# Optimization experiments

Measured on AMD Instinct MI355X. Metric: run time of the kernel, lower is better.

## Reference

```python
import jax, jax.numpy as jnp
import numpy as np

B_IMG = 2
N_PROP = 2000
N_GT = 16
C_FEAT = 256
H_FEAT = 128
W_FEAT = 128
IMG = 1024.0
NUM_CLASSES = 2
BG_THRESH = 0.5          # fg==bg==0.5 -> BETWEEN_THRESHOLDS band is empty
BPI = 512                # batch_size_per_image
NUM_POS_MAX = int(BPI * 0.25)
ENC_W = (1.0, 1.0, 1.0, 1.0, 1.0)
SCALE = 1.0 / 8.0        # feature stride
POOL = 7
SR = 2                   # sampling_ratio
BETA = 1.0 / 9.0
HID = 1024


def _make_boxes(key, shape_prefix, img=IMG):
    kc, ks = jax.random.split(key)
    c = jax.random.uniform(kc, shape_prefix + (2,), minval=0.0, maxval=img)
    s = jax.random.uniform(ks, shape_prefix + (2,), minval=20.0, maxval=200.0)
    lo = jnp.clip(c - 0.5 * s, 0.0, img - 2.0)
    hi = jnp.clip(c + 0.5 * s, lo + 1.0, img)
    return jnp.concatenate([lo, hi], axis=-1)  # [.., x1,y1,x2,y2]


def setup_inputs():
    key = jax.random.key(0)
    ks = jax.random.split(key, 12)
    features = jax.random.normal(ks[0], (B_IMG, C_FEAT, H_FEAT, W_FEAT), dtype=jnp.float32)
    proposals = _make_boxes(ks[1], (B_IMG, N_PROP))
    gt_boxes = _make_boxes(ks[2], (B_IMG, N_GT))
    gt_labels = jax.random.randint(ks[3], (B_IMG, N_GT), 1, NUM_CLASSES, dtype=jnp.int32)
    ka, kb, kt = jax.random.split(ks[4], 3)
    a = jax.random.uniform(ka, (B_IMG, N_GT), minval=10.0, maxval=60.0)
    b = jax.random.uniform(kb, (B_IMG, N_GT), minval=5.0, maxval=30.0)
    th = jax.random.uniform(kt, (B_IMG, N_GT), minval=-np.pi / 2, maxval=np.pi / 2)
    exy = 0.5 * (gt_boxes[..., :2] + gt_boxes[..., 2:])
    gt_ellipses = jnp.stack([a, b, exy[..., 0], exy[..., 1], th], axis=-1)
    d_in = C_FEAT * POOL * POOL
    w1 = jax.random.normal(ks[5], (d_in, HID), dtype=jnp.float32) * 0.02
    b1 = jnp.zeros((HID,), jnp.float32)
    w2 = jax.random.normal(ks[6], (HID, HID), dtype=jnp.float32) * 0.02
    b2 = jnp.zeros((HID,), jnp.float32)
    wc = jax.random.normal(ks[7], (HID, NUM_CLASSES), dtype=jnp.float32) * 0.02
    bc = jnp.zeros((NUM_CLASSES,), jnp.float32)
    wr = jax.random.normal(ks[8], (HID, NUM_CLASSES * 6), dtype=jnp.float32) * 0.02
    br = jnp.zeros((NUM_CLASSES * 6,), jnp.float32)
    return dict(features=features, proposals=proposals, gt_boxes=gt_boxes,
                gt_labels=gt_labels, gt_ellipses=gt_ellipses,
                w1=w1, b1=b1, w2=w2, b2=b2, wc=wc, bc=bc, wr=wr, br=br)


def box_iou(b1, b2):  # [G,4], [P,4] -> [G,P]
    a1 = (b1[:, 2] - b1[:, 0]) * (b1[:, 3] - b1[:, 1])
    a2 = (b2[:, 2] - b2[:, 0]) * (b2[:, 3] - b2[:, 1])
    lt = jnp.maximum(b1[:, None, :2], b2[None, :, :2])
    rb = jnp.minimum(b1[:, None, 2:], b2[None, :, 2:])
    wh = jnp.clip(rb - lt, 0.0)
    inter = wh[..., 0] * wh[..., 1]
    return inter / (a1[:, None] + a2[None, :] - inter)


def encode_ellipses(ell, boxes):  # ell [..,5]=(a,b,cx,cy,theta), boxes [..,4] -> [..,6]
    a, b, ex, ey, th = (ell[..., i] for i in range(5))
    w = jnp.maximum(boxes[..., 2] - boxes[..., 0], 1.0)
    h = jnp.maximum(boxes[..., 3] - boxes[..., 1], 1.0)
    cx = 0.5 * (boxes[..., 0] + boxes[..., 2])
    cy = 0.5 * (boxes[..., 1] + boxes[..., 3])
    wx, wy, wa, wb, wt = ENC_W
    dx = wx * (ex - cx) / w
    dy = wy * (ey - cy) / h
    da = wa * jnp.log(jnp.maximum(2.0 * a, 1e-3) / w)
    db = wb * jnp.log(jnp.maximum(2.0 * b, 1e-3) / h)
    return jnp.stack([dx, dy, da, db, wt * jnp.sin(2.0 * th), wt * jnp.cos(2.0 * th)], axis=-1)


def roi_align(fmap, rois):  # [C,H,W], [R,4] -> [R,C,POOL,POOL]
    C, H, W = fmap.shape
    r = rois * SCALE
    x1, y1, x2, y2 = r[:, 0], r[:, 1], r[:, 2], r[:, 3]
    bw = jnp.maximum(x2 - x1, 1.0) / POOL
    bh = jnp.maximum(y2 - y1, 1.0) / POOL
    S = POOL * SR
    off = (jnp.arange(S, dtype=jnp.float32) + 0.5) / SR  # bin-unit sample offsets
    ys = jnp.clip(y1[:, None] + off[None, :] * bh[:, None], 0.0, H - 1.0)  # [R,S]
    xs = jnp.clip(x1[:, None] + off[None, :] * bw[:, None], 0.0, W - 1.0)
    y0 = jnp.clip(jnp.floor(ys), 0, H - 2).astype(jnp.int32)
    x0 = jnp.clip(jnp.floor(xs), 0, W - 2).astype(jnp.int32)
    ly = ys - y0
    lx = xs - x0
    Ya, Yb = y0[:, :, None], (y0 + 1)[:, :, None]  # [R,S,1]
    Xa, Xb = x0[:, None, :], (x0 + 1)[:, None, :]  # [R,1,S]
    v00 = fmap[:, Ya, Xa]; v01 = fmap[:, Ya, Xb]   # [C,R,S,S]
    v10 = fmap[:, Yb, Xa]; v11 = fmap[:, Yb, Xb]
    wy1 = ly[:, :, None]; wy0 = 1.0 - wy1
    wx1 = lx[:, None, :]; wx0 = 1.0 - wx1
    val = v00 * (wy0 * wx0) + v01 * (wy0 * wx1) + v10 * (wy1 * wx0) + v11 * (wy1 * wx1)
    R = rois.shape[0]
    pooled = val.reshape(C, R, POOL, SR, POOL, SR).mean(axis=(3, 5))
    return pooled.transpose(1, 0, 2, 3)


def reference(features, proposals, gt_boxes, gt_labels, gt_ellipses,
              w1, b1, w2, b2, wc, bc, wr, br):
    B = features.shape[0]
    # add_gt_proposals
    props = jnp.concatenate([proposals, gt_boxes], axis=1)            # [B,P,4]
    # assign_targets_to_proposals: IoU + Matcher (fg=bg=0.5)
    iou = jax.vmap(box_iou)(gt_boxes, props)                          # [B,G,P]
    matched_vals = iou.max(axis=1)
    matches = iou.argmax(axis=1)                                      # [B,P]
    lab = jnp.take_along_axis(gt_labels, matches, axis=1)
    lab = jnp.where(matched_vals < BG_THRESH, 0, lab)                 # background
    # BalancedPositiveNegativeSampler (deterministic, fixed-shape):
    # cap positives at NUM_POS_MAX by random rank, fill rest with random negatives
    rand = jax.random.uniform(jax.random.key(42), lab.shape)
    is_pos = lab > 0
    is_neg = lab == 0
    pos_s = jnp.where(is_pos, rand, -1e9)
    rank = jnp.argsort(jnp.argsort(-pos_s, axis=1), axis=1)
    capped = is_pos & (rank < NUM_POS_MAX)
    prio = jnp.where(capped, rand + 2.0, jnp.where(is_neg, rand, -1e9))
    _, idx = jax.lax.top_k(prio, BPI)                                 # [B,512]
    boxes = jnp.take_along_axis(props, idx[..., None], axis=1)        # [B,512,4]
    labels = jnp.take_along_axis(lab, idx, axis=1)                    # [B,512]
    m = jnp.take_along_axis(matches, idx, axis=1)
    ell = jnp.take_along_axis(gt_ellipses, m[..., None], axis=1)      # [B,512,5]
    targets = encode_ellipses(ell, boxes)                             # [B,512,6]
    # RoIAlign + TwoMLPHead + predictor
    pooled = jax.vmap(roi_align)(features, boxes)                     # [B,512,C,7,7]
    N = B * BPI
    x = pooled.reshape(N, -1)
    x = jax.nn.relu(x @ w1 + b1)
    x = jax.nn.relu(x @ w2 + b2)
    logits = x @ wc + bc                                              # [N,2]
    reg = (x @ wr + br).reshape(N, NUM_CLASSES, 6)
    # ellipse_rcnn_loss
    labels_f = labels.reshape(N)
    t = targets.reshape(N, 6)
    ce = -jnp.take_along_axis(jax.nn.log_softmax(logits, axis=-1), labels_f[:, None], axis=1).mean()
    pred = jnp.take_along_axis(reg, labels_f[:, None, None], axis=1)[:, 0]  # [N,6]
    d = jnp.abs(pred - t)
    sl1 = jnp.where(d < BETA, 0.5 * d * d / BETA, d - 0.5 * BETA)
    reg_loss = jnp.sum(sl1 * (labels_f > 0)[:, None].astype(sl1.dtype)) / N
    return jnp.stack([ce, reg_loss])
```

## Files before the change

### kernel.cpp

```cpp
#include <hip/hip_runtime.h>
#include <hip/hip_bf16.h>
#include <math.h>

#define B_IMG   2
#define N_PROP  2000
#define N_GT    16
#define NPROPS  2016
#define C_FEAT  256
#define H_FEAT  128
#define W_FEAT  128
#define HWF     (H_FEAT*W_FEAT)
#define POOL    7
#define BPI     512
#define NPOSMAX 128
#define NSEL    (B_IMG*BPI)
#define K1      (C_FEAT*POOL*POOL)
#define K1P     12800
#define HID     1024
#define NHEAD   14
#define SPLITK1 8
#define SPLITK2 8

typedef short bf16x8f __attribute__((ext_vector_type(8)));
typedef float f32x4f  __attribute__((ext_vector_type(4)));
typedef short short4v __attribute__((ext_vector_type(4)));

__device__ __forceinline__ void threefry2x32(unsigned k0, unsigned k1,
                                             unsigned& x0, unsigned& x1) {
  unsigned ks[3] = {k0, k1, k0 ^ k1 ^ 0x1BD11BDAu};
  const int R0[4] = {13, 15, 26, 6};
  const int R1[4] = {17, 29, 16, 24};
  x0 += ks[0]; x1 += ks[1];
#pragma unroll
  for (int g = 0; g < 5; g++) {
    const int* rot = (g & 1) ? R1 : R0;
#pragma unroll
    for (int r = 0; r < 4; r++) {
      x0 += x1;
      x1 = (x1 << rot[r]) | (x1 >> (32 - rot[r]));
      x1 ^= x0;
    }
    x0 += ks[(g + 1) % 3];
    x1 += ks[(g + 2) % 3] + (unsigned)(g + 1);
  }
}

#define PRE_SAMPLE   2
#define PRE_TRANS    (PRE_SAMPLE + 2048)
#define PRE_CAST1    (PRE_TRANS + 3136)
#define PRE_CAST0    (PRE_CAST1 + 256)
#define PRE_TOTAL    (PRE_CAST0 + 512)

__global__ __launch_bounds__(256) void k_pre(const float* __restrict__ proposals,
                                             const float* __restrict__ gt_boxes,
                                             const int* __restrict__ gt_labels,
                                             const float* __restrict__ features,
                                             const float* __restrict__ w1,
                                             const float* __restrict__ w2,
                                             float* __restrict__ prio,
                                             int* __restrict__ plab,
                                             int* __restrict__ matches,
                                             __hip_bfloat16* __restrict__ featT,
                                             __hip_bfloat16* __restrict__ W1T,
                                             __hip_bfloat16* __restrict__ W2T,
                                             __hip_bfloat16* __restrict__ Xb) {
  __shared__ __align__(16) char smem[20800];
  int bid = blockIdx.x;
  int tid = threadIdx.x;
  if (bid < PRE_SAMPLE) {
    float* rs    = (float*)smem;
    float* pos_r = (float*)(smem + 8064);
    short* pos_i = (short*)(smem + 16128);
    float* gtb   = (float*)(smem + 20160);
    int*   gtl   = (int*)(smem + 20416);
    int*   cnt   = (int*)(smem + 20480);
    int b = bid;
    int base = b * NPROPS;
    if (tid == 0) *cnt = 0;
    if (tid < N_GT * 4) gtb[tid] = gt_boxes[b * N_GT * 4 + tid];
    if (tid < N_GT) gtl[tid] = gt_labels[b * N_GT + tid];
    __syncthreads();
    for (int i = tid; i < NPROPS; i += 256) {
      unsigned x0 = 0u, x1 = (unsigned)(base + i);
      threefry2x32(0u, 42u, x0, x1);
      unsigned bits = x0 ^ x1;
      float r = __uint_as_float((bits >> 9) | 0x3F800000u) - 1.0f;
      rs[i] = r;
      float p0, p1, p2, p3;
      if (i < N_PROP) {
        const float4 v = *(const float4*)(proposals + ((size_t)b * N_PROP + i) * 4);
        p0 = v.x; p1 = v.y; p2 = v.z; p3 = v.w;
      } else {
        const float* g = &gtb[(i - N_PROP) * 4];
        p0 = g[0]; p1 = g[1]; p2 = g[2]; p3 = g[3];
      }
      float a2 = (p2 - p0) * (p3 - p1);
      float best = -1.0f; int bg = 0;
#pragma unroll
      for (int g = 0; g < N_GT; g++) {
        float g0 = gtb[g*4], g1 = gtb[g*4+1], g2 = gtb[g*4+2], g3 = gtb[g*4+3];
        float a1 = (g2 - g0) * (g3 - g1);
        float wx = fmaxf(fminf(g2, p2) - fmaxf(g0, p0), 0.0f);
        float wy = fmaxf(fminf(g3, p3) - fmaxf(g1, p1), 0.0f);
        float inter = wx * wy;
        float iou = inter / (a1 + a2 - inter);
        if (iou > best) { best = iou; bg = g; }
      }
      matches[base + i] = bg;
      int lab = (best < 0.5f) ? 0 : gtl[bg];
      plab[base + i] = lab;
      if (lab > 0) {
        int s = atomicAdd(cnt, 1);
        pos_i[s] = (short)i; pos_r[s] = r;
      }
    }
    __syncthreads();
    int P = *cnt;
    for (int s = tid; s < P; s += 256) {
      int i = pos_i[s]; float ri = pos_r[s];
      int ch = 0;
      for (int j = 0; j < P; j++) {
        float rj = pos_r[j]; int ij = pos_i[j];
        ch += (rj > ri || (rj == ri && ij < i)) ? 1 : 0;
      }
      rs[i] = (ch < NPOSMAX) ? (ri + 2.0f) : -1000000000.0f;
    }
    __syncthreads();
    for (int i = tid; i < NPROPS; i += 256) prio[base + i] = rs[i];
  } else if (bid < PRE_TRANS) {
    float (*tile)[65] = (float(*)[65])smem;
    int t = bid - PRE_SAMPLE;
    int b = t >> 10;
    int rem = t & 1023;
    int c0 = (rem >> 8) * 64;
    int s0 = (rem & 255) * 64;
    const float* src = features + (size_t)b * C_FEAT * HWF;
    __hip_bfloat16* dst = featT + (size_t)b * HWF * C_FEAT;
    int hw4 = (tid & 15) * 4, cr = tid >> 4;
#pragma unroll
    for (int p = 0; p < 4; p++) {
      int c = cr + p * 16;
      float4 v = *(const float4*)(src + (size_t)(c0 + c) * HWF + s0 + hw4);
      tile[hw4 + 0][c] = v.x; tile[hw4 + 1][c] = v.y;
      tile[hw4 + 2][c] = v.z; tile[hw4 + 3][c] = v.w;
    }
    __syncthreads();
    int c4 = (tid & 15) * 4, hr = tid >> 4;
#pragma unroll
    for (int p = 0; p < 4; p++) {
      int hw = hr + p * 16;
      __hip_bfloat16 o[4] = {__float2bfloat16(tile[hw][c4]), __float2bfloat16(tile[hw][c4+1]),
                             __float2bfloat16(tile[hw][c4+2]), __float2bfloat16(tile[hw][c4+3])};
      *(short4v*)(dst + (size_t)(s0 + hw) * C_FEAT + c0 + c4) = *(short4v*)o;
    }
  } else if (bid < PRE_CAST1) {
    float (*tile)[65] = (float(*)[65])smem;
    int t = bid - PRE_TRANS;
    int p = t >> 6;
    int rem = t & 63;
    int c0 = (rem & 3) * 64;
    int n0 = (rem >> 2) * 64;
    int n4 = (tid & 15) * 4, ig = tid >> 4;
#pragma unroll
    for (int i = ig; i < 64; i += 16) {
      float4 v = *(const float4*)(w1 + (size_t)((c0 + i) * 49 + p) * HID + n0 + n4);
      tile[i][n4] = v.x; tile[i][n4 + 1] = v.y;
      tile[i][n4 + 2] = v.z; tile[i][n4 + 3] = v.w;
    }
    __syncthreads();
    int c4 = (tid & 15) * 4;
#pragma unroll
    for (int i = ig; i < 64; i += 16) {
      __hip_bfloat16 o[4] = {__float2bfloat16(tile[c4][i]), __float2bfloat16(tile[c4 + 1][i]),
                             __float2bfloat16(tile[c4 + 2][i]), __float2bfloat16(tile[c4 + 3][i])};
      *(short4v*)(W1T + (size_t)(n0 + i) * K1P + p * 256 + c0 + c4) = *(short4v*)o;
    }
  } else if (bid < PRE_CAST0) {
    float (*tile)[65] = (float(*)[65])smem;
    int t = bid - PRE_CAST1;
    int c0 = (t & 15) * 64;
    int n0 = (t >> 4) * 64;
    int n4 = (tid & 15) * 4, ig = tid >> 4;
#pragma unroll
    for (int i = ig; i < 64; i += 16) {
      float4 v = *(const float4*)(w2 + (size_t)(c0 + i) * HID + n0 + n4);
      tile[i][n4] = v.x; tile[i][n4 + 1] = v.y;
      tile[i][n4 + 2] = v.z; tile[i][n4 + 3] = v.w;
    }
    __syncthreads();
    int c4 = (tid & 15) * 4;
#pragma unroll
    for (int i = ig; i < 64; i += 16) {
      __hip_bfloat16 o[4] = {__float2bfloat16(tile[c4][i]), __float2bfloat16(tile[c4 + 1][i]),
                             __float2bfloat16(tile[c4 + 2][i]), __float2bfloat16(tile[c4 + 3][i])};
      *(short4v*)(W2T + (size_t)(n0 + i) * HID + c0 + c4) = *(short4v*)o;
    }
  } else {
    int t = bid - PRE_CAST0;
    __hip_bfloat16* buf = (t >> 8) ? W1T : Xb;
    int tt = (t & 255) * 256 + tid;
    int row = tt >> 6;
    int col4 = (tt & 63) << 2;
    short4v z = {0, 0, 0, 0};
    *(short4v*)(buf + (size_t)row * K1P + K1 + col4) = z;
  }
}

__global__ __launch_bounds__(256) void k_select(const float* __restrict__ prio,
    const float* __restrict__ proposals, const float* __restrict__ gt_boxes,
    const int* __restrict__ matches, const int* __restrict__ plab,
    const float* __restrict__ gt_ell,
    float* __restrict__ sel_boxes, int* __restrict__ sel_labels,
    float* __restrict__ targets) {
  int tid = threadIdx.x;
  int wave = tid >> 6, lane = tid & 63;
  int b = blockIdx.y;
  int base = b * NPROPS;
  int i = blockIdx.x * 4 + wave;
  float pi = prio[base + i];
  int rank = 0;
  for (int j = lane; j < NPROPS; j += 64) {
    float pj = prio[base + j];
    rank += (pj > pi || (pj == pi && j < i)) ? 1 : 0;
  }
#pragma unroll
  for (int off = 32; off > 0; off >>= 1) rank += __shfl_down(rank, off);
  if (lane != 0 || rank >= BPI) return;
  int slot = b * BPI + rank;
  float p0, p1, p2, p3;
  if (i < N_PROP) {
    const float* p = proposals + ((size_t)b * N_PROP + i) * 4;
    p0 = p[0]; p1 = p[1]; p2 = p[2]; p3 = p[3];
  } else {
    const float* p = gt_boxes + ((size_t)b * N_GT + (i - N_PROP)) * 4;
    p0 = p[0]; p1 = p[1]; p2 = p[2]; p3 = p[3];
  }
  sel_boxes[slot * 4 + 0] = p0;
  sel_boxes[slot * 4 + 1] = p1;
  sel_boxes[slot * 4 + 2] = p2;
  sel_boxes[slot * 4 + 3] = p3;
  int lb = plab[base + i];
  sel_labels[slot] = lb;
  int m = matches[base + i];
  const float* e = gt_ell + ((size_t)b * N_GT + m) * 5;
  float ea = e[0], eb = e[1], ex = e[2], ey = e[3], eth = e[4];
  float w = fmaxf(p2 - p0, 1.0f), h = fmaxf(p3 - p1, 1.0f);
  float cx = 0.5f * (p0 + p2), cy = 0.5f * (p1 + p3);
  float* t = targets + (size_t)slot * 6;
  t[0] = (ex - cx) / w;
  t[1] = (ey - cy) / h;
  t[2] = logf(fmaxf(2.0f * ea, 0.001f) / w);
  t[3] = logf(fmaxf(2.0f * eb, 0.001f) / h);
  t[4] = sinf(2.0f * eth);
  t[5] = cosf(2.0f * eth);
}

__global__ __launch_bounds__(256) void k_roialign(const __hip_bfloat16* __restrict__ featT,
                                                  const float* __restrict__ sel_boxes,
                                                  __hip_bfloat16* __restrict__ X) {
  int n = blockIdx.x;
  int py = blockIdx.y;
  int t = threadIdx.x;
  int lane = t & 63, sub = t >> 6;
  int c = lane << 2;
  int b = n >> 9;
  const float* bx = sel_boxes + (size_t)n * 4;
  float x1 = bx[0] * 0.125f, y1 = bx[1] * 0.125f;
  float x2 = bx[2] * 0.125f, y2 = bx[3] * 0.125f;
  float bw = fmaxf(x2 - x1, 1.0f) / 7.0f;
  float bh = fmaxf(y2 - y1, 1.0f) / 7.0f;
  const __hip_bfloat16* base = featT + (size_t)b * HWF * C_FEAT;
  int y0A[2]; float lyA[2];
#pragma unroll
  for (int sy = 0; sy < 2; sy++) {
    float off = ((float)(py * 2 + sy) + 0.5f) * 0.5f;
    float ys = fminf(fmaxf(y1 + off * bh, 0.0f), 127.0f);
    int y0 = (int)fminf(fmaxf(floorf(ys), 0.0f), 126.0f);
    y0A[sy] = y0; lyA[sy] = ys - (float)y0;
  }
#pragma unroll
  for (int pass = 0; pass < 2; pass++) {
    int px = sub + (pass << 2);
    if (px >= 7) break;
    float acc[4] = {0.0f, 0.0f, 0.0f, 0.0f};
#pragma unroll
    for (int sx = 0; sx < 2; sx++) {
      float off = ((float)(px * 2 + sx) + 0.5f) * 0.5f;
      float xs = fminf(fmaxf(x1 + off * bw, 0.0f), 127.0f);
      int x0 = (int)fminf(fmaxf(floorf(xs), 0.0f), 126.0f);
      float lx = xs - (float)x0;
#pragma unroll
      for (int sy = 0; sy < 2; sy++) {
        int y0 = y0A[sy]; float ly = lyA[sy];
        const __hip_bfloat16* p = base + ((size_t)(y0 * W_FEAT + x0)) * C_FEAT + c;
        short4v s00 = *(const short4v*)p;
        short4v s01 = *(const short4v*)(p + C_FEAT);
        short4v s10 = *(const short4v*)(p + W_FEAT * C_FEAT);
        short4v s11 = *(const short4v*)(p + W_FEAT * C_FEAT + C_FEAT);
        float w00 = (1.0f - ly) * (1.0f - lx), w01 = (1.0f - ly) * lx;
        float w10 = ly * (1.0f - lx), w11 = ly * lx;
#pragma unroll
        for (int q = 0; q < 4; q++) {
          float v00 = __uint_as_float(((unsigned)(unsigned short)s00[q]) << 16);
          float v01 = __uint_as_float(((unsigned)(unsigned short)s01[q]) << 16);
          float v10 = __uint_as_float(((unsigned)(unsigned short)s10[q]) << 16);
          float v11 = __uint_as_float(((unsigned)(unsigned short)s11[q]) << 16);
          acc[q] += v00 * w00 + v01 * w01 + v10 * w10 + v11 * w11;
        }
      }
    }
    __hip_bfloat16 o[4] = {__float2bfloat16(acc[0] * 0.25f), __float2bfloat16(acc[1] * 0.25f),
                           __float2bfloat16(acc[2] * 0.25f), __float2bfloat16(acc[3] * 0.25f)};
    *(short4v*)&X[(size_t)n * K1P + (size_t)(py * 7 + px) * C_FEAT + c] = *(short4v*)o;
  }
}

__device__ __forceinline__ void gld_lds16(const __hip_bfloat16* g, __hip_bfloat16* l) {
  __builtin_amdgcn_global_load_lds(
      (const __attribute__((address_space(1))) void*)g,
      (__attribute__((address_space(3))) void*)l, 16, 0, 0);
}

#define G1_KC   1600
#define G1_NKT  25
#define G1_ABUF 16384
#define G1_BUFE 24576

__global__ __launch_bounds__(512, 1) void k_gemm1(const __hip_bfloat16* __restrict__ A,
                                                  const __hip_bfloat16* __restrict__ BT,
                                                  __hip_bfloat16* __restrict__ Pb) {
  __shared__ __align__(16) __hip_bfloat16 lds[3 * G1_BUFE];
  const int lin = blockIdx.x;
  const int kz = lin >> 5;
  const int q  = lin & 31;
  const int m0 = (q >> 3) * 256;
  const int n0 = (q & 7) * 128;
  const int kbeg = kz * G1_KC;
  const int tid = threadIdx.x;
  const int wave = tid >> 6, lane = tid & 63;
  const int wm = (wave & 3) * 64, wn = (wave >> 2) * 64;
  const int lm = lane & 15, quad = lane >> 4;

  f32x4f acc[4][4] = {};

  auto stage = [&](int kt, int sb) {
    const int kcol = kbeg + kt * 64;
    __hip_bfloat16* lb = lds + sb * G1_BUFE;
#pragma unroll
    for (int u = 0; u < 4; ++u) {
      int idx = tid + u * 512;
      int r = idx >> 3, g = (idx & 7) ^ (r & 7);
      gld_lds16(A + (size_t)(m0 + r) * K1P + kcol + g * 8, lb + idx * 8);
    }
#pragma unroll
    for (int u = 0; u < 2; ++u) {
      int idx = tid + u * 512;
      int r = idx >> 3, g = (idx & 7) ^ (r & 7);
      gld_lds16(BT + (size_t)(n0 + r) * K1P + kcol + g * 8, lb + G1_ABUF + idx * 8);
    }
  };

  stage(0, 0);
  stage(1, 1);
  asm volatile("s_waitcnt vmcnt(6)" ::: "memory");
  __builtin_amdgcn_s_barrier();

  int buf = 0;
  for (int kt = 0; kt < G1_NKT; ++kt) {
    int sb = buf + 2; if (sb >= 3) sb -= 3;
    if (kt + 2 < G1_NKT) stage(kt + 2, sb);
    const __hip_bfloat16* Ab = lds + buf * G1_BUFE;
    const __hip_bfloat16* Bb = Ab + G1_ABUF;
    bf16x8f af[4][2], bf[4][2];
#pragma unroll
    for (int i = 0; i < 4; ++i)
#pragma unroll
      for (int s = 0; s < 2; ++s)
        af[i][s] = *(const bf16x8f*)(Ab + (wm + i * 16 + lm) * 64 +
                                     (((s << 2) + quad) ^ (lm & 7)) * 8);
#pragma unroll
    for (int j = 0; j < 4; ++j)
#pragma unroll
      for (int s = 0; s < 2; ++s)
        bf[j][s] = *(const bf16x8f*)(Bb + (wn + j * 16 + lm) * 64 +
                                     (((s << 2) + quad) ^ (lm & 7)) * 8);
    __builtin_amdgcn_s_setprio(1);
#pragma unroll
    for (int s = 0; s < 2; ++s)
#pragma unroll
      for (int i = 0; i < 4; ++i)
#pragma unroll
        for (int j = 0; j < 4; ++j)
          acc[i][j] = __builtin_amdgcn_mfma_f32_16x16x32_bf16(af[i][s], bf[j][s], acc[i][j], 0, 0, 0);
    __builtin_amdgcn_s_setprio(0);
    if (kt < G1_NKT - 1) {
      if (kt < G1_NKT - 2) asm volatile("s_waitcnt vmcnt(6)" ::: "memory");
      else                 asm volatile("s_waitcnt vmcnt(0)" ::: "memory");
      __builtin_amdgcn_s_barrier();
    }
    buf = (buf == 2) ? 0 : buf + 1;
  }

  int tileoff = ((m0 >> 8) * 8 + (n0 >> 7)) * 32768;
  __hip_bfloat16* dst = Pb + ((size_t)kz << 20) + tileoff + wave * 4096 + lane * 4;
#pragma unroll
  for (int i = 0; i < 4; ++i)
#pragma unroll
    for (int j = 0; j < 4; ++j) {
      __hip_bfloat16 o[4] = {__float2bfloat16(acc[i][j][0]), __float2bfloat16(acc[i][j][1]),
                             __float2bfloat16(acc[i][j][2]), __float2bfloat16(acc[i][j][3])};
      *(short4v*)(dst + (i * 4 + j) * 256) = *(short4v*)o;
    }
}

template <int MODE>
__global__ __launch_bounds__(MODE == 1 ? 512 : 256)
void k_mfma_gemm(const __hip_bfloat16* __restrict__ A,
                 const __hip_bfloat16* __restrict__ BT,
                 __hip_bfloat16* __restrict__ Pb, int K, int KC) {
  const int AM  = (MODE == 1) ? 256 : 128;
  const int TPB = AM * 2;
  __shared__ __align__(16) __hip_bfloat16 As[AM * 32];
  __shared__ __align__(16) __hip_bfloat16 Bs[128 * 32];
  int lin = blockIdx.x;
  int n0, m0, kz;
  if (MODE == 1) {
    int c = lin & 7, h = lin >> 8, qq = (lin >> 3) & 31;
    kz = c + (h << 3);
    n0 = (qq & 7) * 128;
    m0 = (qq >> 3) * 256;
  } else {
    kz = lin & 7;
    int qq = lin >> 3;
    n0 = (qq & 7) * 128;
    m0 = (qq >> 3) * 128;
  }
  int tid = threadIdx.x;
  int kbeg = kz * KC;
  int srow = tid >> 2;
  int scs  = tid & 3;
  int sg   = scs ^ (srow & 3);
  int scol = sg << 3;
  int wave = tid >> 6, lane = tid & 63;
  const int WMW = AM / 64;
  int wm = (wave % WMW) * 64, wn = (wave / WMW) * 64;
  int lm = lane & 15, quad = lane >> 4;
  int fco = ((quad ^ (lm & 3)) << 3);
  f32x4f acc[4][4] = {};
  for (int k0 = kbeg; k0 < kbeg + KC; k0 += 32) {
    __syncthreads();
#pragma unroll
    for (int r0 = 0; r0 < AM; r0 += TPB / 4)
      gld_lds16(A + (size_t)(m0 + r0 + srow) * K + k0 + scol, &As[(r0 + srow) * 32 + scs * 8]);
#pragma unroll
    for (int r0 = 0; r0 < 128; r0 += TPB / 4)
      gld_lds16(BT + (size_t)(n0 + r0 + srow) * K + k0 + scol, &Bs[(r0 + srow) * 32 + scs * 8]);
    __syncthreads();
    bf16x8f af[4], bf[4];
#pragma unroll
    for (int i = 0; i < 4; i++)
      af[i] = *(const bf16x8f*)&As[(wm + i * 16 + lm) * 32 + fco];
#pragma unroll
    for (int j = 0; j < 4; j++)
      bf[j] = *(const bf16x8f*)&Bs[(wn + j * 16 + lm) * 32 + fco];
#pragma unroll
    for (int i = 0; i < 4; i++)
#pragma unroll
      for (int j = 0; j < 4; j++)
        acc[i][j] = __builtin_amdgcn_mfma_f32_16x16x32_bf16(af[i], bf[j], acc[i][j], 0, 0, 0);
  }
  int tileoff = (MODE == 1) ? (((m0 >> 8) * 8 + (n0 >> 7)) * 32768)
                            : (((m0 >> 7) * 8 + (n0 >> 7)) * 16384);
  __hip_bfloat16* dst = Pb + ((size_t)kz << 20) + tileoff + wave * 4096 + lane * 4;
#pragma unroll
  for (int i = 0; i < 4; i++)
#pragma unroll
    for (int j = 0; j < 4; j++) {
      __hip_bfloat16 o[4] = {__float2bfloat16(acc[i][j][0]), __float2bfloat16(acc[i][j][1]),
                             __float2bfloat16(acc[i][j][2]), __float2bfloat16(acc[i][j][3])};
      *(short4v*)(dst + (i * 4 + j) * 256) = *(short4v*)o;
    }
}

__global__ __launch_bounds__(256) void k_reduce16(const __hip_bfloat16* __restrict__ Pb,
                                                  const float* __restrict__ bias,
                                                  __hip_bfloat16* __restrict__ O) {
  int m4 = blockIdx.x >> 2;
  int n  = (blockIdx.x & 3) * 256 + threadIdx.x;
  int m0i = m4 >> 6, wavem = (m4 >> 4) & 3, i = (m4 >> 2) & 3, quad = m4 & 3;
  int n0i = n >> 7, wn = (n >> 6) & 1, j = (n >> 4) & 3, lm = n & 15;
  int wave = wavem + wn * 4;
  int elem = (m0i * 8 + n0i) * 32768 + wave * 4096 + (i * 4 + j) * 256 + (quad * 16 + lm) * 4;
  float s0 = 0.0f, s1 = 0.0f, s2 = 0.0f, s3 = 0.0f;
#pragma unroll
  for (int z = 0; z < SPLITK1; z++) {
    short4v v = *(const short4v*)(Pb + ((size_t)z << 20) + elem);
    s0 += __uint_as_float(((unsigned)(unsigned short)v[0]) << 16);
    s1 += __uint_as_float(((unsigned)(unsigned short)v[1]) << 16);
    s2 += __uint_as_float(((unsigned)(unsigned short)v[2]) << 16);
    s3 += __uint_as_float(((unsigned)(unsigned short)v[3]) << 16);
  }
  float bv = bias[n];
  int m = m4 * 4;
  O[(size_t)(m + 0) * HID + n] = __float2bfloat16(fmaxf(s0 + bv, 0.0f));
  O[(size_t)(m + 1) * HID + n] = __float2bfloat16(fmaxf(s1 + bv, 0.0f));
  O[(size_t)(m + 2) * HID + n] = __float2bfloat16(fmaxf(s2 + bv, 0.0f));
  O[(size_t)(m + 3) * HID + n] = __float2bfloat16(fmaxf(s3 + bv, 0.0f));
}

__global__ __launch_bounds__(256) void k_reduce_head(const __hip_bfloat16* __restrict__ Pb,
                                                     const float* __restrict__ bias,
                                                     const float* __restrict__ wc,
                                                     const float* __restrict__ bc,
                                                     const float* __restrict__ wr,
                                                     const float* __restrict__ br,
                                                     float* __restrict__ Y) {
  __shared__ float part[4][NHEAD];
  int m = blockIdx.x, tid = threadIdx.x;
  int m0i = m >> 7, wavem = (m >> 6) & 1, fi = (m >> 4) & 3, quad = (m >> 2) & 3, r = m & 3;
  float a[NHEAD];
#pragma unroll
  for (int j = 0; j < NHEAD; j++) a[j] = 0.0f;
#pragma unroll
  for (int nn = 0; nn < 4; nn++) {
    int n = nn * 256 + tid;
    int n0i = n >> 7, wn = (n >> 6) & 1, fj = (n >> 4) & 3, lm = n & 15;
    int wave = wavem + wn * 2;
    int elem = (m0i * 8 + n0i) * 16384 + wave * 4096 + (fi * 4 + fj) * 256
             + (quad * 16 + lm) * 4 + r;
    float s = 0.0f;
#pragma unroll
    for (int z = 0; z < SPLITK2; z++)
      s += __uint_as_float(((unsigned)*(const unsigned short*)(Pb + ((size_t)z << 20) + elem)) << 16);
    float hv = fmaxf(s + bias[n], 0.0f);
    float2 wcv = *(const float2*)(wc + n * 2);
    float4 w0 = *(const float4*)(wr + n * 12);
    float4 w1 = *(const float4*)(wr + n * 12 + 4);
    float4 w2 = *(const float4*)(wr + n * 12 + 8);
    a[0] += hv * wcv.x;  a[1] += hv * wcv.y;
    a[2] += hv * w0.x;   a[3] += hv * w0.y;  a[4] += hv * w0.z;  a[5] += hv * w0.w;
    a[6] += hv * w1.x;   a[7] += hv * w1.y;  a[8] += hv * w1.z;  a[9] += hv * w1.w;
    a[10] += hv * w2.x;  a[11] += hv * w2.y; a[12] += hv * w2.z; a[13] += hv * w2.w;
  }
#pragma unroll
  for (int j = 0; j < NHEAD; j++)
#pragma unroll
    for (int off = 32; off > 0; off >>= 1) a[j] += __shfl_down(a[j], off);
  int wave = tid >> 6, lane = tid & 63;
  if (lane == 0)
#pragma unroll
    for (int j = 0; j < NHEAD; j++) part[wave][j] = a[j];
  __syncthreads();
  if (tid < NHEAD) {
    float v = part[0][tid] + part[1][tid] + part[2][tid] + part[3][tid];
    Y[(size_t)m * NHEAD + tid] = v + ((tid < 2) ? bc[tid] : br[tid - 2]);
  }
}

__global__ __launch_bounds__(1024) void k_loss(const float* __restrict__ Y,
                                               const int* __restrict__ sel_labels,
                                               const float* __restrict__ T,
                                               float* __restrict__ out) {
  __shared__ float sc[1024];
  __shared__ float sr[1024];
  int n = threadIdx.x;
  float l0 = Y[(size_t)n * NHEAD + 0], l1 = Y[(size_t)n * NHEAD + 1];
  int lb = sel_labels[n];
  float mx = fmaxf(l0, l1);
  float lse = mx + logf(expf(l0 - mx) + expf(l1 - mx));
  float ce = lse - (lb ? l1 : l0);
  float reg = 0.0f;
  if (lb > 0) {
    const float beta = 1.0f / 9.0f;
    const float* pr = Y + (size_t)n * NHEAD + 2 + lb * 6;
    const float* t = T + (size_t)n * 6;
#pragma unroll
    for (int j = 0; j < 6; j++) {
      float d = fabsf(pr[j] - t[j]);
      reg += (d < beta) ? (0.5f * d * d / beta) : (d - 0.5f * beta);
    }
  }
  sc[n] = ce; sr[n] = reg;
  __syncthreads();
  for (int s = 512; s > 0; s >>= 1) {
    if (n < s) { sc[n] += sc[n + s]; sr[n] += sr[n + s]; }
    __syncthreads();
  }
  if (n == 0) {
    out[0] = sc[0] * (1.0f / 1024.0f);
    out[1] = sr[0] * (1.0f / 1024.0f);
  }
}

extern "C" void kernel_launch(void* const* d_in, const int* in_sizes, int n_in,
                              void* d_out, int out_size, void* d_ws, size_t ws_size,
                              hipStream_t stream) {
  const float* features  = (const float*)d_in[0];
  const float* proposals = (const float*)d_in[1];
  const float* gt_boxes  = (const float*)d_in[2];
  const int*   gt_labels = (const int*)d_in[3];
  const float* gt_ell    = (const float*)d_in[4];
  const float* w1 = (const float*)d_in[5];
  const float* b1 = (const float*)d_in[6];
  const float* w2 = (const float*)d_in[7];
  const float* b2 = (const float*)d_in[8];
  const float* wc = (const float*)d_in[9];
  const float* bc = (const float*)d_in[10];
  const float* wr = (const float*)d_in[11];
  const float* br = (const float*)d_in[12];
  float* out = (float*)d_out;

  char* ws = (char*)d_ws;
  size_t off = 0;
  auto take = [&](size_t bytes) -> void* {
    void* p = ws + off;
    off = (off + bytes + 255) & ~(size_t)255;
    return p;
  };
  __hip_bfloat16* Pb = (__hip_bfloat16*)take((size_t)16 * (1 << 20) * 2);
  __hip_bfloat16* featT = Pb;
  __hip_bfloat16* Xb  = (__hip_bfloat16*)take((size_t)NSEL * K1P * 2);
  float* Y = (float*)Xb;
  __hip_bfloat16* W1T = (__hip_bfloat16*)take((size_t)HID * K1P * 2);
  __hip_bfloat16* W2T = (__hip_bfloat16*)take((size_t)HID * HID * 2);
  __hip_bfloat16* H1b = (__hip_bfloat16*)take((size_t)NSEL * HID * 2);
  int*   matches   = (int*)take((size_t)B_IMG * NPROPS * 4);
  int*   plab      = (int*)take((size_t)B_IMG * NPROPS * 4);
  float* prio      = (float*)take((size_t)B_IMG * NPROPS * 4);
  float* sel_boxes = (float*)take((size_t)NSEL * 4 * 4);
  int*   sel_lab   = (int*)take((size_t)NSEL * 4);
  float* targets   = (float*)take((size_t)NSEL * 6 * 4);

  k_pre<<<PRE_TOTAL, 256, 0, stream>>>(proposals, gt_boxes, gt_labels, features,
                                       w1, w2, prio, plab, matches,
                                       featT, W1T, W2T, Xb);
  k_select<<<dim3(NPROPS / 4, B_IMG), 256, 0, stream>>>(prio, proposals, gt_boxes,
                                                        matches, plab, gt_ell,
                                                        sel_boxes, sel_lab, targets);
  k_roialign<<<dim3(NSEL, POOL), 256, 0, stream>>>(featT, sel_boxes, Xb);

  k_gemm1<<<256, 512, 0, stream>>>(Xb, W1T, Pb);
  k_reduce16<<<1024, 256, 0, stream>>>(Pb, b1, H1b);
  k_mfma_gemm<2><<<512, 256, 0, stream>>>(H1b, W2T, Pb, HID, HID / SPLITK2);
  k_reduce_head<<<1024, 256, 0, stream>>>(Pb, b2, wc, bc, wr, br, Y);

  k_loss<<<1, 1024, 0, stream>>>(Y, sel_lab, targets, out);
}
```

Measured before the change: 245.6 us.

## Widen RoIAlign loads, remap gemm1 block order, fuse loss into head reduce

RoIAlign now has each thread handle 8 channels with 16-byte loads and stores, one pooled column per 32-thread group, instead of two passes of 4 channels. The gemm1 block index mapping is permuted so that consecutive blocks share the same N tile across M tiles and K splits, aiming for better L2 reuse of the weight tile. The separate single-block loss kernel is removed: the last head-reduce block to finish, detected with an atomic counter, computes the loss. This saves one launch but adds a serial tail on one block, and the counter is never reset, so correctness relies on a modulo check across repeated calls.

```diff
diff --git a/kernel.cpp b/kernel.cpp
--- a/kernel.cpp
+++ b/kernel.cpp
@@ -261,14 +261,16 @@
   int n = blockIdx.x;
   int py = blockIdx.y;
   int t = threadIdx.x;
-  int lane = t & 63, sub = t >> 6;
-  int c = lane << 2;
+  int px = t >> 5;
+  int lane32 = t & 31;
+  int c = lane32 << 3;
   int b = n >> 9;
   const float* bx = sel_boxes + (size_t)n * 4;
   float x1 = bx[0] * 0.125f, y1 = bx[1] * 0.125f;
   float x2 = bx[2] * 0.125f, y2 = bx[3] * 0.125f;
   float bw = fmaxf(x2 - x1, 1.0f) / 7.0f;
   float bh = fmaxf(y2 - y1, 1.0f) / 7.0f;
+  if (px >= 7) return;
   const __hip_bfloat16* base = featT + (size_t)b * HWF * C_FEAT;
   int y0A[2]; float lyA[2];
 #pragma unroll
@@ -278,41 +280,37 @@
     int y0 = (int)fminf(fmaxf(floorf(ys), 0.0f), 126.0f);
     y0A[sy] = y0; lyA[sy] = ys - (float)y0;
   }
-#pragma unroll
-  for (int pass = 0; pass < 2; pass++) {
-    int px = sub + (pass << 2);
-    if (px >= 7) break;
-    float acc[4] = {0.0f, 0.0f, 0.0f, 0.0f};
-#pragma unroll
-    for (int sx = 0; sx < 2; sx++) {
-      float off = ((float)(px * 2 + sx) + 0.5f) * 0.5f;
-      float xs = fminf(fmaxf(x1 + off * bw, 0.0f), 127.0f);
-      int x0 = (int)fminf(fmaxf(floorf(xs), 0.0f), 126.0f);
-      float lx = xs - (float)x0;
-#pragma unroll
-      for (int sy = 0; sy < 2; sy++) {
-        int y0 = y0A[sy]; float ly = lyA[sy];
-        const __hip_bfloat16* p = base + ((size_t)(y0 * W_FEAT + x0)) * C_FEAT + c;
-        short4v s00 = *(const short4v*)p;
-        short4v s01 = *(const short4v*)(p + C_FEAT);
-        short4v s10 = *(const short4v*)(p + W_FEAT * C_FEAT);
-        short4v s11 = *(const short4v*)(p + W_FEAT * C_FEAT + C_FEAT);
-        float w00 = (1.0f - ly) * (1.0f - lx), w01 = (1.0f - ly) * lx;
-        float w10 = ly * (1.0f - lx), w11 = ly * lx;
-#pragma unroll
-        for (int q = 0; q < 4; q++) {
-          float v00 = __uint_as_float(((unsigned)(unsigned short)s00[q]) << 16);
-          float v01 = __uint_as_float(((unsigned)(unsigned short)s01[q]) << 16);
-          float v10 = __uint_as_float(((unsigned)(unsigned short)s10[q]) << 16);
-          float v11 = __uint_as_float(((unsigned)(unsigned short)s11[q]) << 16);
-          acc[q] += v00 * w00 + v01 * w01 + v10 * w10 + v11 * w11;
-        }
+  float acc[8] = {};
+#pragma unroll
+  for (int sx = 0; sx < 2; sx++) {
+    float off = ((float)(px * 2 + sx) + 0.5f) * 0.5f;
+    float xs = fminf(fmaxf(x1 + off * bw, 0.0f), 127.0f);
+    int x0 = (int)fminf(fmaxf(floorf(xs), 0.0f), 126.0f);
+    float lx = xs - (float)x0;
+#pragma unroll
+    for (int sy = 0; sy < 2; sy++) {
+      int y0 = y0A[sy]; float ly = lyA[sy];
+      const __hip_bfloat16* p = base + ((size_t)(y0 * W_FEAT + x0)) * C_FEAT + c;
+      bf16x8f s00 = *(const bf16x8f*)p;
+      bf16x8f s01 = *(const bf16x8f*)(p + C_FEAT);
+      bf16x8f s10 = *(const bf16x8f*)(p + W_FEAT * C_FEAT);
+      bf16x8f s11 = *(const bf16x8f*)(p + W_FEAT * C_FEAT + C_FEAT);
+      float w00 = (1.0f - ly) * (1.0f - lx), w01 = (1.0f - ly) * lx;
+      float w10 = ly * (1.0f - lx), w11 = ly * lx;
+#pragma unroll
+      for (int q = 0; q < 8; q++) {
+        float v00 = __uint_as_float(((unsigned)(unsigned short)s00[q]) << 16);
+        float v01 = __uint_as_float(((unsigned)(unsigned short)s01[q]) << 16);
+        float v10 = __uint_as_float(((unsigned)(unsigned short)s10[q]) << 16);
+        float v11 = __uint_as_float(((unsigned)(unsigned short)s11[q]) << 16);
+        acc[q] += v00 * w00 + v01 * w01 + v10 * w10 + v11 * w11;
       }
     }
-    __hip_bfloat16 o[4] = {__float2bfloat16(acc[0] * 0.25f), __float2bfloat16(acc[1] * 0.25f),
-                           __float2bfloat16(acc[2] * 0.25f), __float2bfloat16(acc[3] * 0.25f)};
-    *(short4v*)&X[(size_t)n * K1P + (size_t)(py * 7 + px) * C_FEAT + c] = *(short4v*)o;
-  }
+  }
+  __hip_bfloat16 o[8];
+#pragma unroll
+  for (int q = 0; q < 8; q++) o[q] = __float2bfloat16(acc[q] * 0.25f);
+  *(bf16x8f*)&X[(size_t)n * K1P + (size_t)(py * 7 + px) * C_FEAT + c] = *(bf16x8f*)o;
 }
 
 __device__ __forceinline__ void gld_lds16(const __hip_bfloat16* g, __hip_bfloat16* l) {
@@ -331,10 +329,10 @@
                                                   __hip_bfloat16* __restrict__ Pb) {
   __shared__ __align__(16) __hip_bfloat16 lds[3 * G1_BUFE];
   const int lin = blockIdx.x;
-  const int kz = lin >> 5;
-  const int q  = lin & 31;
-  const int m0 = (q >> 3) * 256;
-  const int n0 = (q & 7) * 128;
+  const int pair = (lin & 7) + ((lin >> 6) << 3);
+  const int m0 = (pair & 3) * 256;
+  const int kz = pair >> 2;
+  const int n0 = ((lin >> 3) & 7) * 128;
   const int kbeg = kz * G1_KC;
   const int tid = threadIdx.x;
   const int wave = tid >> 6, lane = tid & 63;
@@ -514,8 +512,14 @@
                                                      const float* __restrict__ bc,
                                                      const float* __restrict__ wr,
                                                      const float* __restrict__ br,
-                                                     float* __restrict__ Y) {
+                                                     float* __restrict__ Y,
+                                                     const int* __restrict__ sel_labels,
+                                                     const float* __restrict__ T,
+                                                     float* __restrict__ out,
+                                                     int* __restrict__ loss_cnt) {
   __shared__ float part[4][NHEAD];
+  __shared__ int lastf;
+  __shared__ float rcs[4], rrs[4];
   int m = blockIdx.x, tid = threadIdx.x;
   int m0i = m >> 7, wavem = (m >> 6) & 1, fi = (m >> 4) & 3, quad = (m >> 2) & 3, r = m & 3;
   float a[NHEAD];
@@ -555,40 +559,45 @@
     float v = part[0][tid] + part[1][tid] + part[2][tid] + part[3][tid];
     Y[(size_t)m * NHEAD + tid] = v + ((tid < 2) ? bc[tid] : br[tid - 2]);
   }
-}
-
-__global__ __launch_bounds__(1024) void k_loss(const float* __restrict__ Y,
-                                               const int* __restrict__ sel_labels,
-                                               const float* __restrict__ T,
-                                               float* __restrict__ out) {
-  __shared__ float sc[1024];
-  __shared__ float sr[1024];
-  int n = threadIdx.x;
-  float l0 = Y[(size_t)n * NHEAD + 0], l1 = Y[(size_t)n * NHEAD + 1];
-  int lb = sel_labels[n];
-  float mx = fmaxf(l0, l1);
-  float lse = mx + logf(expf(l0 - mx) + expf(l1 - mx));
-  float ce = lse - (lb ? l1 : l0);
-  float reg = 0.0f;
-  if (lb > 0) {
-    const float beta = 1.0f / 9.0f;
-    const float* pr = Y + (size_t)n * NHEAD + 2 + lb * 6;
-    const float* t = T + (size_t)n * 6;
-#pragma unroll
-    for (int j = 0; j < 6; j++) {
-      float d = fabsf(pr[j] - t[j]);
-      reg += (d < beta) ? (0.5f * d * d / beta) : (d - 0.5f * beta);
-    }
-  }
-  sc[n] = ce; sr[n] = reg;
   __syncthreads();
-  for (int s = 512; s > 0; s >>= 1) {
-    if (n < s) { sc[n] += sc[n + s]; sr[n] += sr[n + s]; }
-    __syncthreads();
-  }
-  if (n == 0) {
-    out[0] = sc[0] * (1.0f / 1024.0f);
-    out[1] = sr[0] * (1.0f / 1024.0f);
+  if (tid == 0) {
+    __threadfence();
+    int old = atomicAdd(loss_cnt, 1);
+    lastf = ((old & 1023) == 1023) ? 1 : 0;
+  }
+  __syncthreads();
+  if (!lastf) return;
+  __threadfence();
+  float ce_s = 0.0f, rg_s = 0.0f;
+#pragma unroll
+  for (int k2 = 0; k2 < 4; k2++) {
+    int s = tid + k2 * 256;
+    float l0 = Y[(size_t)s * NHEAD + 0], l1 = Y[(size_t)s * NHEAD + 1];
+    int lb = sel_labels[s];
+    float mx = fmaxf(l0, l1);
+    float lse = mx + logf(expf(l0 - mx) + expf(l1 - mx));
+    ce_s += lse - (lb ? l1 : l0);
+    if (lb > 0) {
+      const float beta = 1.0f / 9.0f;
+      const float* pr = Y + (size_t)s * NHEAD + 2 + lb * 6;
+      const float* tt = T + (size_t)s * 6;
+#pragma unroll
+      for (int j = 0; j < 6; j++) {
+        float d = fabsf(pr[j] - tt[j]);
+        rg_s += (d < beta) ? (0.5f * d * d / beta) : (d - 0.5f * beta);
+      }
+    }
+  }
+#pragma unroll
+  for (int off = 32; off > 0; off >>= 1) {
+    ce_s += __shfl_down(ce_s, off);
+    rg_s += __shfl_down(rg_s, off);
+  }
+  if (lane == 0) { rcs[wave] = ce_s; rrs[wave] = rg_s; }
+  __syncthreads();
+  if (tid == 0) {
+    out[0] = (rcs[0] + rcs[1] + rcs[2] + rcs[3]) * (1.0f / 1024.0f);
+    out[1] = (rrs[0] + rrs[1] + rrs[2] + rrs[3]) * (1.0f / 1024.0f);
   }
 }
 
@@ -630,6 +639,7 @@
   float* sel_boxes = (float*)take((size_t)NSEL * 4 * 4);
   int*   sel_lab   = (int*)take((size_t)NSEL * 4);
   float* targets   = (float*)take((size_t)NSEL * 6 * 4);
+  int*   loss_cnt  = (int*)take(256);
 
   k_pre<<<PRE_TOTAL, 256, 0, stream>>>(proposals, gt_boxes, gt_labels, features,
                                        w1, w2, prio, plab, matches,
@@ -642,7 +652,6 @@
   k_gemm1<<<256, 512, 0, stream>>>(Xb, W1T, Pb);
   k_reduce16<<<1024, 256, 0, stream>>>(Pb, b1, H1b);
   k_mfma_gemm<2><<<512, 256, 0, stream>>>(H1b, W2T, Pb, HID, HID / SPLITK2);
-  k_reduce_head<<<1024, 256, 0, stream>>>(Pb, b2, wc, bc, wr, br, Y);
-
-  k_loss<<<1, 1024, 0, stream>>>(Y, sel_lab, targets, out);
-}
+  k_reduce_head<<<1024, 256, 0, stream>>>(Pb, b2, wc, bc, wr, br, Y,
+                                          sel_lab, targets, out, loss_cnt);
+}
```

Result: slower. 257.6 us (+4.9%).
